# Performance work log

Hardware: AMD Instinct MI355X
Metric: run time of the kernel (lower is better)

The kernel has to match this reference:

```python
import jax, jax.numpy as jnp
import numpy as np

E, C, D, F = 8, 2048, 2048, 8192  # experts, capacity/expert, d_model, d_ff

def setup_inputs() -> dict:
    key = jax.random.key(0)
    ks = jax.random.split(key, 5)
    s_in = 1.0 / np.sqrt(D)
    s_h = 1.0 / np.sqrt(F)
    return {
        "inputs": jax.random.normal(ks[0], (1, E * C, D), dtype=jnp.float32),
        "w1": jax.random.normal(ks[1], (E, D, F), dtype=jnp.float32) * s_in,
        "b1": jax.random.normal(ks[2], (E, F), dtype=jnp.float32) * 0.01,
        "w2": jax.random.normal(ks[3], (E, F, D), dtype=jnp.float32) * s_h,
        "b2": jax.random.normal(ks[4], (E, D), dtype=jnp.float32) * 0.01,
    }

def reference(inputs, w1, b1, w2, b2):
    # inputs: [G, E*C, D]; chunk along dim=1 == reshape to [G, E, C, D]
    G, T, d = inputs.shape
    x = inputs.reshape(G, E, T // E, d)
    # grouped FFN: per-expert Linear -> GELU(exact, torch default) -> Linear
    h = jnp.einsum('gecd,edf->gecf', x, w1) + b1[None, :, None, :]
    h = jax.nn.gelu(h, approximate=False)
    y = jnp.einsum('gecf,efd->gecd', h, w2) + b2[None, :, None, :]
    # torch.cat(expert_outputs, dim=1) == reshape back
    return y.reshape(G, T, d)
```

## Files before the change

### kernel.cpp

```cpp
#include <hip/hip_runtime.h>
#include <hip/hip_bf16.h>


#define E_ 8
#define C_ 2048
#define D_ 2048
#define F_ 8192

typedef short bf16x8 __attribute__((ext_vector_type(8)));
typedef float f32x4  __attribute__((ext_vector_type(4)));

__device__ inline unsigned short f2bf(float f) {
    unsigned u = __float_as_uint(f);
    u += 0x7fffu + ((u >> 16) & 1u);
    return (unsigned short)(u >> 16);
}

__device__ inline float gelu_fast(float x) {
    float z = 0.7978845608028654f * (x + 0.044715f * x * x * x);
    float e = __expf(-2.0f * fabsf(z));
    float t = (1.0f - e) / (1.0f + e);
    t = copysignf(t, z);
    return 0.5f * x * (1.0f + t);
}

__device__ inline void gload_lds16(const void* g, void* l) {
    __builtin_amdgcn_global_load_lds(
        (const __attribute__((address_space(1))) void*)g,
        (__attribute__((address_space(3))) void*)l, 16, 0, 0);
}

__global__ __launch_bounds__(256) void cvt_kernel(
    const float* __restrict__ in, unsigned short* __restrict__ out, long n4)
{
    long i = (long)blockIdx.x * 256 + threadIdx.x;
    if (i >= n4) return;
    float4 v = ((const float4*)in)[i];
    union { unsigned short u[4]; uint2 q; } r;
    r.u[0] = f2bf(v.x); r.u[1] = f2bf(v.y); r.u[2] = f2bf(v.z); r.u[3] = f2bf(v.w);
    ((uint2*)out)[i] = r.q;
}

__global__ __launch_bounds__(256) void transpose_cvt(
    const float* __restrict__ in, unsigned short* __restrict__ out,
    int R, int Cc, int RT, int CT)
{
    __shared__ float lds[64][65];
    int bx = blockIdx.x;
    int e  = bx / (RT * CT);
    int rem = bx % (RT * CT);
    int rt = rem / CT, ct = rem % CT;
    const float* ine = in + (long)e * R * Cc;
    unsigned short* oute = out + (long)e * R * Cc;
    long r0 = (long)rt * 64, c0 = (long)ct * 64;
    int t = threadIdx.x;

    int lr = t >> 4, lc = t & 15;
#pragma unroll
    for (int ii = 0; ii < 4; ++ii) {
        int r = lr + ii * 16;
        float4 v = *(const float4*)(ine + (r0 + r) * Cc + c0 + lc * 4);
        lds[r][lc * 4 + 0] = v.x; lds[r][lc * 4 + 1] = v.y;
        lds[r][lc * 4 + 2] = v.z; lds[r][lc * 4 + 3] = v.w;
    }
    __syncthreads();

    int nl = t >> 3, kv = t & 7;
#pragma unroll
    for (int ii = 0; ii < 2; ++ii) {
        int n = nl + ii * 32;
        union { unsigned short u[8]; uint4 q; } r;
#pragma unroll
        for (int j = 0; j < 8; ++j) r.u[j] = f2bf(lds[kv * 8 + j][n]);
        *(uint4*)(oute + (c0 + n) * R + r0 + kv * 8) = r.q;
    }
}

#define REG_A0 0
#define REG_A1 16384
#define REG_B0 32768
#define REG_B1 49152
#define SLOT_B 65536

#define MFMA16(d, a, b) d = __builtin_amdgcn_mfma_f32_16x16x32_bf16(a, b, d, 0, 0, 0)

template <bool GELU, bool OUT_BF16>
__global__ __launch_bounds__(512, 2) void gemm8p(
    const unsigned short* __restrict__ A,
    const unsigned short* __restrict__ Bt,
    const float* __restrict__ bias,
    void* __restrict__ Cout,
    int M, int N, int K,
    long strideAe, long strideBe, long strideCe, int biasStride)
{
    extern __shared__ char ldsb[];

    constexpr int BM = 256, BN = 256, BK = 64;
    int MT = M / BM, NT = N / BN;
    int nwg = gridDim.x;
    int bid = blockIdx.x;
    int tile = (nwg % 8 == 0) ? (bid % 8) * (nwg / 8) + bid / 8 : bid;
    int e   = tile / (MT * NT);
    int rem = tile % (MT * NT);
    int mt = rem / NT, nt = rem % NT;

    const unsigned short* Ae = A  + (long)e * strideAe + (long)mt * BM * K;
    const unsigned short* Be = Bt + (long)e * strideBe + (long)nt * BN * K;

    int tid = threadIdx.x, lane = tid & 63, wid = tid >> 6;
    int wr = wid >> 2, wc = wid & 3;

    auto stage_region = [&](const unsigned short* base, int ktile, int kreg, int dstByte) {
        long k0 = (long)ktile * BK + kreg * 32;
#pragma unroll
        for (int i = 0; i < 2; ++i) {
            int g   = wid * 128 + i * 64 + lane;
            int row = g >> 2, col = g & 3;
            int sw  = col ^ ((row >> 1) & 3);
            gload_lds16(base + (long)row * K + k0 + sw * 8, ldsb + dstByte + g * 16);
        }
    };

    f32x4 acc[8][4] = {};
    int KT = K / BK;

    int rbaseA = wr * 128 + (lane & 15);
    int rbaseB = wc * 64  + (lane & 15);
    int kq = lane >> 4;

    stage_region(Ae, 0, 0, REG_A0);
    stage_region(Be, 0, 0, REG_B0);
    stage_region(Ae, 0, 1, REG_A1);
    stage_region(Be, 0, 1, REG_B1);
    stage_region(Ae, 1, 0, SLOT_B + REG_A0);
    stage_region(Be, 1, 0, SLOT_B + REG_B0);
    stage_region(Ae, 1, 1, SLOT_B + REG_A1);

    for (int T = 0; T < KT; ++T) {
        int so = (T & 1) * SLOT_B;

        if (T == KT - 1) asm volatile("s_waitcnt vmcnt(0)" ::: "memory");
        else             asm volatile("s_waitcnt vmcnt(6)" ::: "memory");
        __builtin_amdgcn_sched_barrier(0);
        __builtin_amdgcn_s_barrier();
        __builtin_amdgcn_sched_barrier(0);

        bf16x8 a0[8], b0[4];
#pragma unroll
        for (int m = 0; m < 8; ++m) {
            int row = rbaseA + m * 16;
            a0[m] = *(const bf16x8*)(ldsb + so + REG_A0 + row * 64 + ((kq ^ ((row >> 1) & 3)) << 4));
        }
#pragma unroll
        for (int n = 0; n < 4; ++n) {
            int row = rbaseB + n * 16;
            b0[n] = *(const bf16x8*)(ldsb + so + REG_B0 + row * 64 + ((kq ^ ((row >> 1) & 3)) << 4));
        }
        if (T + 1 < KT) stage_region(Be, T + 1, 1, (so ^ SLOT_B) + REG_B1);
        __builtin_amdgcn_s_barrier();
        __builtin_amdgcn_s_setprio(1);
#pragma unroll
        for (int m = 0; m < 8; ++m) { MFMA16(acc[m][0], a0[m], b0[0]); MFMA16(acc[m][1], a0[m], b0[1]); }
        __builtin_amdgcn_s_setprio(0);
        __builtin_amdgcn_s_barrier();

        if (T + 2 < KT) stage_region(Ae, T + 2, 0, so + REG_A0);
        __builtin_amdgcn_s_barrier();
        __builtin_amdgcn_s_setprio(1);
#pragma unroll
        for (int m = 0; m < 8; ++m) { MFMA16(acc[m][2], a0[m], b0[2]); MFMA16(acc[m][3], a0[m], b0[3]); }
        __builtin_amdgcn_s_setprio(0);
        __builtin_amdgcn_s_barrier();

        bf16x8 a1[8], b1[4];
#pragma unroll
        for (int m = 0; m < 8; ++m) {
            int row = rbaseA + m * 16;
            a1[m] = *(const bf16x8*)(ldsb + so + REG_A1 + row * 64 + ((kq ^ ((row >> 1) & 3)) << 4));
        }
#pragma unroll
        for (int n = 0; n < 4; ++n) {
            int row = rbaseB + n * 16;
            b1[n] = *(const bf16x8*)(ldsb + so + REG_B1 + row * 64 + ((kq ^ ((row >> 1) & 3)) << 4));
        }
        if (T + 2 < KT) stage_region(Be, T + 2, 0, so + REG_B0);
        __builtin_amdgcn_s_barrier();
        __builtin_amdgcn_s_setprio(1);
#pragma unroll
        for (int m = 0; m < 8; ++m) { MFMA16(acc[m][0], a1[m], b1[0]); MFMA16(acc[m][1], a1[m], b1[1]); }
        __builtin_amdgcn_s_setprio(0);
        __builtin_amdgcn_s_barrier();

        if (T + 2 < KT) stage_region(Ae, T + 2, 1, so + REG_A1);
        __builtin_amdgcn_s_barrier();
        __builtin_amdgcn_s_setprio(1);
#pragma unroll
        for (int m = 0; m < 8; ++m) { MFMA16(acc[m][2], a1[m], b1[2]); MFMA16(acc[m][3], a1[m], b1[3]); }
        __builtin_amdgcn_s_setprio(0);
        __builtin_amdgcn_s_barrier();
    }

    const float* be = bias + (long)e * biasStride + nt * BN;
    long cBase = (long)e * strideCe + ((long)mt * BM) * N + (long)nt * BN;
#pragma unroll
    for (int m = 0; m < 8; ++m) {
#pragma unroll
        for (int n = 0; n < 4; ++n) {
            int col = wc * 64 + n * 16 + (lane & 15);
            float bv = be[col];
#pragma unroll
            for (int j = 0; j < 4; ++j) {
                int row = wr * 128 + m * 16 + (lane >> 4) * 4 + j;
                float v = acc[m][n][j] + bv;
                if (GELU) v = gelu_fast(v);
                long idx = cBase + (long)row * N + col;
                if (OUT_BF16) ((unsigned short*)Cout)[idx] = f2bf(v);
                else          ((float*)Cout)[idx] = v;
            }
        }
    }
}

extern "C" void kernel_launch(void* const* d_in, const int* in_sizes, int n_in,
                              void* d_out, int out_size, void* d_ws, size_t ws_size,
                              hipStream_t stream)
{
    const float* x  = (const float*)d_in[0];
    const float* w1 = (const float*)d_in[1];
    const float* b1 = (const float*)d_in[2];
    const float* w2 = (const float*)d_in[3];
    const float* b2 = (const float*)d_in[4];
    float* out = (float*)d_out;

    (void)hipFuncSetAttribute((const void*)gemm8p<true, true>,
                              hipFuncAttributeMaxDynamicSharedMemorySize, 131072);
    (void)hipFuncSetAttribute((const void*)gemm8p<false, false>,
                              hipFuncAttributeMaxDynamicSharedMemorySize, 131072);

    const long CD = (long)C_ * D_;
    const long DF = (long)D_ * F_;
    const long CF = (long)C_ * F_;
    const long perExpertElems = CD + 2 * DF + CF;
    long ceMax = (long)(ws_size / ((size_t)perExpertElems * 2));
    int CE = (int)(ceMax < 1 ? 1 : (ceMax > E_ ? E_ : ceMax));

    unsigned short* xb  = (unsigned short*)d_ws;
    unsigned short* w1t = xb  + (long)CE * CD;
    unsigned short* w2t = w1t + (long)CE * DF;
    unsigned short* h   = w2t + (long)CE * DF;

    for (int e0 = 0; e0 < E_; e0 += CE) {
        int ce = (E_ - e0) < CE ? (E_ - e0) : CE;

        long n4 = (long)ce * CD / 4;
        cvt_kernel<<<(int)((n4 + 255) / 256), 256, 0, stream>>>(
            x + (long)e0 * CD, xb, n4);

        transpose_cvt<<<ce * (D_ / 64) * (F_ / 64), 256, 0, stream>>>(
            w1 + (long)e0 * DF, w1t, D_, F_, D_ / 64, F_ / 64);

        transpose_cvt<<<ce * (F_ / 64) * (D_ / 64), 256, 0, stream>>>(
            w2 + (long)e0 * DF, w2t, F_, D_, F_ / 64, D_ / 64);

        gemm8p<true, true><<<ce * (C_ / 256) * (F_ / 256), 512, 131072, stream>>>(
            xb, w1t, b1 + (long)e0 * F_, (void*)h,
            C_, F_, D_, CD, DF, CF, F_);

        gemm8p<false, false><<<ce * (C_ / 256) * (D_ / 256), 512, 131072, stream>>>(
            h, w2t, b2 + (long)e0 * D_, (void*)(out + (long)e0 * CD),
            C_, D_, F_, CF, DF, CD, D_);
    }
}
```

Before: 1.527 ms.

## Restructure GEMM k-loop into 2x2 quadrant MFMA phases and group tiles by N

Reorders the inner GEMM loop so each phase reads both k-halves of a 4x2 sub-block of A/B fragments from LDS, then issues its MFMAs. Each phase ends with an explicit lgkmcnt(0) fence. Global-to-LDS prefetches are redistributed among the phases, and staging offsets are precomputed once per thread. Work-group tiles are also remapped so groups of four N-tiles are walked along M, aimed at better L2 reuse of weights. The changes target LDS read latency and cache locality, at the cost of extra waits, different register pressure and a riskier prefetch-ordering invariant.

```diff
diff --git a/kernel.cpp b/kernel.cpp
--- a/kernel.cpp
+++ b/kernel.cpp
@@ -83,6 +83,9 @@
 #define SLOT_B 65536
 
 #define MFMA16(d, a, b) d = __builtin_amdgcn_mfma_f32_16x16x32_bf16(a, b, d, 0, 0, 0)
+#define LGKM0_FENCE() do { \
+    asm volatile("s_waitcnt lgkmcnt(0)" ::: "memory"); \
+    __builtin_amdgcn_sched_barrier(0); } while (0)
 
 template <bool GELU, bool OUT_BF16>
 __global__ __launch_bounds__(512, 2) void gemm8p(
@@ -95,14 +98,17 @@
 {
     extern __shared__ char ldsb[];
 
-    constexpr int BM = 256, BN = 256, BK = 64;
+    constexpr int BM = 256, BN = 256, BK = 64, GRP = 4;
     int MT = M / BM, NT = N / BN;
+    int per = MT * NT;
     int nwg = gridDim.x;
     int bid = blockIdx.x;
-    int tile = (nwg % 8 == 0) ? (bid % 8) * (nwg / 8) + bid / 8 : bid;
-    int e   = tile / (MT * NT);
-    int rem = tile % (MT * NT);
-    int mt = rem / NT, nt = rem % NT;
+    int tile = (nwg % 8 == 0) ? (bid & 7) * (nwg >> 3) + (bid >> 3) : bid;
+    int e = tile / per, s = tile % per;
+    int ng  = s / (MT * GRP);
+    int r2  = s % (MT * GRP);
+    int mt  = r2 >> 2;
+    int nt  = ng * GRP + (r2 & 3);
 
     const unsigned short* Ae = A  + (long)e * strideAe + (long)mt * BM * K;
     const unsigned short* Be = Bt + (long)e * strideBe + (long)nt * BN * K;
@@ -110,15 +116,17 @@
     int tid = threadIdx.x, lane = tid & 63, wid = tid >> 6;
     int wr = wid >> 2, wc = wid & 3;
 
+    int g0 = wid * 128 + lane, g1 = g0 + 64;
+    long sOff0, sOff1; int sDst0, sDst1;
+    { int row = g0 >> 2, col = g0 & 3, sw = col ^ ((row >> 1) & 3);
+      sOff0 = (long)row * K + sw * 8; sDst0 = g0 * 16; }
+    { int row = g1 >> 2, col = g1 & 3, sw = col ^ ((row >> 1) & 3);
+      sOff1 = (long)row * K + sw * 8; sDst1 = g1 * 16; }
+
     auto stage_region = [&](const unsigned short* base, int ktile, int kreg, int dstByte) {
         long k0 = (long)ktile * BK + kreg * 32;
-#pragma unroll
-        for (int i = 0; i < 2; ++i) {
-            int g   = wid * 128 + i * 64 + lane;
-            int row = g >> 2, col = g & 3;
-            int sw  = col ^ ((row >> 1) & 3);
-            gload_lds16(base + (long)row * K + k0 + sw * 8, ldsb + dstByte + g * 16);
-        }
+        gload_lds16(base + sOff0 + k0, ldsb + dstByte + sDst0);
+        gload_lds16(base + sOff1 + k0, ldsb + dstByte + sDst1);
     };
 
     f32x4 acc[8][4] = {};
@@ -127,6 +135,17 @@
     int rbaseA = wr * 128 + (lane & 15);
     int rbaseB = wc * 64  + (lane & 15);
     int kq = lane >> 4;
+
+    auto rdA = [&](int so, int ks, int m) -> bf16x8 {
+        int row = rbaseA + m * 16;
+        return *(const bf16x8*)(ldsb + so + (ks ? REG_A1 : REG_A0)
+                                + row * 64 + ((kq ^ ((row >> 1) & 3)) << 4));
+    };
+    auto rdB = [&](int so, int ks, int n) -> bf16x8 {
+        int row = rbaseB + n * 16;
+        return *(const bf16x8*)(ldsb + so + (ks ? REG_B1 : REG_B0)
+                                + row * 64 + ((kq ^ ((row >> 1) & 3)) << 4));
+    };
 
     stage_region(Ae, 0, 0, REG_A0);
     stage_region(Be, 0, 0, REG_B0);
@@ -136,6 +155,8 @@
     stage_region(Be, 1, 0, SLOT_B + REG_B0);
     stage_region(Ae, 1, 1, SLOT_B + REG_A1);
 
+    bf16x8 a[8][2], b[4][2];
+
     for (int T = 0; T < KT; ++T) {
         int so = (T & 1) * SLOT_B;
 
@@ -145,57 +166,68 @@
         __builtin_amdgcn_s_barrier();
         __builtin_amdgcn_sched_barrier(0);
 
-        bf16x8 a0[8], b0[4];
-#pragma unroll
-        for (int m = 0; m < 8; ++m) {
-            int row = rbaseA + m * 16;
-            a0[m] = *(const bf16x8*)(ldsb + so + REG_A0 + row * 64 + ((kq ^ ((row >> 1) & 3)) << 4));
+        #pragma unroll
+        for (int m = 0; m < 4; ++m) { a[m][0] = rdA(so, 0, m); a[m][1] = rdA(so, 1, m); }
+        #pragma unroll
+        for (int n = 0; n < 2; ++n) { b[n][0] = rdB(so, 0, n); b[n][1] = rdB(so, 1, n); }
+        if (T + 1 < KT) stage_region(Be, T + 1, 1, (so ^ SLOT_B) + REG_B1);
+        __builtin_amdgcn_s_barrier();
+        LGKM0_FENCE();
+        __builtin_amdgcn_s_setprio(1);
+        #pragma unroll
+        for (int m = 0; m < 4; ++m)
+            #pragma unroll
+            for (int n = 0; n < 2; ++n) {
+                MFMA16(acc[m][n], a[m][0], b[n][0]);
+                MFMA16(acc[m][n], a[m][1], b[n][1]);
+            }
+        __builtin_amdgcn_s_setprio(0);
+        __builtin_amdgcn_s_barrier();
+
+        #pragma unroll
+        for (int n = 2; n < 4; ++n) { b[n][0] = rdB(so, 0, n); b[n][1] = rdB(so, 1, n); }
+        __builtin_amdgcn_s_barrier();
+        LGKM0_FENCE();
+        __builtin_amdgcn_s_setprio(1);
+        #pragma unroll
+        for (int m = 0; m < 4; ++m)
+            #pragma unroll
+            for (int n = 2; n < 4; ++n) {
+                MFMA16(acc[m][n], a[m][0], b[n][0]);
+                MFMA16(acc[m][n], a[m][1], b[n][1]);
+            }
+        __builtin_amdgcn_s_setprio(0);
+        __builtin_amdgcn_s_barrier();
+
+        #pragma unroll
+        for (int m = 4; m < 8; ++m) { a[m][0] = rdA(so, 0, m); a[m][1] = rdA(so, 1, m); }
+        if (T + 2 < KT) stage_region(Be, T + 2, 0, so + REG_B0);
+        __builtin_amdgcn_s_barrier();
+        LGKM0_FENCE();
+        __builtin_amdgcn_s_setprio(1);
+        #pragma unroll
+        for (int m = 4; m < 8; ++m)
+            #pragma unroll
+            for (int n = 0; n < 2; ++n) {
+                MFMA16(acc[m][n], a[m][0], b[n][0]);
+                MFMA16(acc[m][n], a[m][1], b[n][1]);
+            }
+        __builtin_amdgcn_s_setprio(0);
+        __builtin_amdgcn_s_barrier();
+
+        if (T + 2 < KT) {
+            stage_region(Ae, T + 2, 0, so + REG_A0);
+            stage_region(Ae, T + 2, 1, so + REG_A1);
         }
-#pragma unroll
-        for (int n = 0; n < 4; ++n) {
-            int row = rbaseB + n * 16;
-            b0[n] = *(const bf16x8*)(ldsb + so + REG_B0 + row * 64 + ((kq ^ ((row >> 1) & 3)) << 4));
-        }
-        if (T + 1 < KT) stage_region(Be, T + 1, 1, (so ^ SLOT_B) + REG_B1);
         __builtin_amdgcn_s_barrier();
         __builtin_amdgcn_s_setprio(1);
-#pragma unroll
-        for (int m = 0; m < 8; ++m) { MFMA16(acc[m][0], a0[m], b0[0]); MFMA16(acc[m][1], a0[m], b0[1]); }
-        __builtin_amdgcn_s_setprio(0);
-        __builtin_amdgcn_s_barrier();
-
-        if (T + 2 < KT) stage_region(Ae, T + 2, 0, so + REG_A0);
-        __builtin_amdgcn_s_barrier();
-        __builtin_amdgcn_s_setprio(1);
-#pragma unroll
-        for (int m = 0; m < 8; ++m) { MFMA16(acc[m][2], a0[m], b0[2]); MFMA16(acc[m][3], a0[m], b0[3]); }
-        __builtin_amdgcn_s_setprio(0);
-        __builtin_amdgcn_s_barrier();
-
-        bf16x8 a1[8], b1[4];
-#pragma unroll
-        for (int m = 0; m < 8; ++m) {
-            int row = rbaseA + m * 16;
-            a1[m] = *(const bf16x8*)(ldsb + so + REG_A1 + row * 64 + ((kq ^ ((row >> 1) & 3)) << 4));
-        }
-#pragma unroll
-        for (int n = 0; n < 4; ++n) {
-            int row = rbaseB + n * 16;
-            b1[n] = *(const bf16x8*)(ldsb + so + REG_B1 + row * 64 + ((kq ^ ((row >> 1) & 3)) << 4));
-        }
-        if (T + 2 < KT) stage_region(Be, T + 2, 0, so + REG_B0);
-        __builtin_amdgcn_s_barrier();
-        __builtin_amdgcn_s_setprio(1);
-#pragma unroll
-        for (int m = 0; m < 8; ++m) { MFMA16(acc[m][0], a1[m], b1[0]); MFMA16(acc[m][1], a1[m], b1[1]); }
-        __builtin_amdgcn_s_setprio(0);
-        __builtin_amdgcn_s_barrier();
-
-        if (T + 2 < KT) stage_region(Ae, T + 2, 1, so + REG_A1);
-        __builtin_amdgcn_s_barrier();
-        __builtin_amdgcn_s_setprio(1);
-#pragma unroll
-        for (int m = 0; m < 8; ++m) { MFMA16(acc[m][2], a1[m], b1[2]); MFMA16(acc[m][3], a1[m], b1[3]); }
+        #pragma unroll
+        for (int m = 4; m < 8; ++m)
+            #pragma unroll
+            for (int n = 2; n < 4; ++n) {
+                MFMA16(acc[m][n], a[m][0], b[n][0]);
+                MFMA16(acc[m][n], a[m][1], b[n][1]);
+            }
         __builtin_amdgcn_s_setprio(0);
         __builtin_amdgcn_s_barrier();
     }
```

Measured after the change: 1.476 ms. 1.03x faster.
